# Kernel optimization log

Measured on AMD Instinct MI355X. Metric: run time of the kernel, lower is better.

## Reference

```python
import jax, jax.numpy as jnp
import numpy as np

KERNEL = (9, 9, 9)  # box-filter window
KSIZE = KERNEL[0] * KERNEL[1] * KERNEL[2]  # 729
GAMMA = 1.0


def _box_sum(x):
    # x: [B, C, D, H, W] -> channel-sum then 9x9x9 sliding-window sum (SAME pad),
    # exactly matching F.conv3d with an all-ones [1, C, 9,9,9] kernel, pad=4.
    s = jnp.sum(x, axis=1, keepdims=True)  # [B,1,D,H,W]
    return jax.lax.reduce_window(
        s, jnp.asarray(0.0, s.dtype), jax.lax.add,
        window_dimensions=(1, 1) + KERNEL,
        window_strides=(1, 1, 1, 1, 1),
        padding='SAME')


def setup_inputs() -> dict:
    key = jax.random.key(0)
    k1, k2, k3 = jax.random.split(key, 3)
    shape = (2, 1, 160, 160, 160)
    return {
        'input': jax.random.normal(k1, shape, dtype=jnp.float32),
        'target': jax.random.normal(k2, shape, dtype=jnp.float32),
        'flow': jax.random.normal(k3, shape, dtype=jnp.float32),
    }


def reference(input, target, flow):
    # normalize target from (-1, 1) to (0, 1)
    target = (target + 1.0) * 0.5
    w = jax.nn.sigmoid(flow) ** GAMMA  # voxel-wise confidence weight

    T_sum = _box_sum(target)
    I_sum = _box_sum(input)
    TT_sum = _box_sum(target * target)
    II_sum = _box_sum(input * input)
    IT_sum = _box_sum(input * target)

    Ihat = I_sum / KSIZE
    That = T_sum / KSIZE
    cross = IT_sum - Ihat * T_sum - That * I_sum + That * Ihat * KSIZE
    T_var = TT_sum - 2.0 * That * T_sum + That * That * KSIZE
    I_var = II_sum - 2.0 * Ihat * I_sum + Ihat * Ihat * KSIZE

    cc = cross * cross * w / (T_var * I_var + 1e-5)
    return -1.0 * jnp.mean(cc)
```

## Files before the change

### kernel.cpp

```cpp
#include <hip/hip_runtime.h>


constexpr int NB = 2;
constexpr int ND = 160;
constexpr int NH = 160;
constexpr int NW = 160;
constexpr int TH = 16;
constexpr int TW = 16;
constexpr int DCHUNK = 32;
constexpr int NDCH = ND / DCHUNK;
constexpr float INV_K = 1.0f / 729.0f;
constexpr double INV_COUNT = 1.0 / (double(NB) * ND * NH * NW);

__device__ __forceinline__ void compute_plane(
    const float* __restrict__ in, const float* __restrict__ tg,
    int b, int dp, int h0, int w0, int tid,
    float* __restrict__ inT, float* __restrict__ tgT,
    float* __restrict__ tmp5, float* __restrict__ Pbuf)
{
    if (tid < 144) {
        int r = tid / 6;
        int q = tid - r * 6;
        int gh = h0 - 4 + r;
        int gw = w0 - 4 + q * 4;
        float4 iv = make_float4(0.f, 0.f, 0.f, 0.f);
        float4 tv = make_float4(0.f, 0.f, 0.f, 0.f);
        if (((unsigned)gh < (unsigned)NH) && ((unsigned)gw < (unsigned)NW)) {
            long base = ((long)((b * ND + dp) * NH + gh)) * NW + gw;
            iv = *reinterpret_cast<const float4*>(in + base);
            float4 rv = *reinterpret_cast<const float4*>(tg + base);
            tv.x = fmaf(rv.x, 0.5f, 0.5f);
            tv.y = fmaf(rv.y, 0.5f, 0.5f);
            tv.z = fmaf(rv.z, 0.5f, 0.5f);
            tv.w = fmaf(rv.w, 0.5f, 0.5f);
        }
        reinterpret_cast<float4*>(inT)[r * 6 + q] = iv;
        reinterpret_cast<float4*>(tgT)[r * 6 + q] = tv;
    }
    __syncthreads();

    {
        int pos = tid;
        #pragma unroll
        for (int rep = 0; rep < 2; ++rep) {
            if (pos < 384) {
                int r = pos >> 4, wo = pos & 15;
                const float* ir = inT + r * 24 + wo;
                const float* tr = tgT + r * 24 + wo;
                float s0 = 0.f, s1 = 0.f, s2 = 0.f, s3 = 0.f, s4 = 0.f;
                #pragma unroll
                for (int k = 0; k < 9; ++k) {
                    float ivv = ir[k];
                    float t = tr[k];
                    s0 += t;
                    s1 += ivv;
                    s2 = fmaf(t, t, s2);
                    s3 = fmaf(ivv, ivv, s3);
                    s4 = fmaf(ivv, t, s4);
                }
                int o = r * 16 + wo;
                tmp5[0 * 384 + o] = s0;
                tmp5[1 * 384 + o] = s1;
                tmp5[2 * 384 + o] = s2;
                tmp5[3 * 384 + o] = s3;
                tmp5[4 * 384 + o] = s4;
            }
            pos += 256;
        }
    }
    __syncthreads();

    if (tid < 80) {
        int f = tid >> 4, w = tid & 15;
        const float* basep = tmp5 + f * 384 + w;
        float s = 0.f;
        #pragma unroll
        for (int r = 0; r < 8; ++r) s += basep[r * 16];
        #pragma unroll
        for (int ho = 0; ho < 16; ++ho) {
            s += basep[(ho + 8) * 16];
            Pbuf[f * 256 + ho * 16 + w] = s;
            s -= basep[ho * 16];
        }
    }
    __syncthreads();
}

__global__ void __launch_bounds__(256)
cc3d_main(const float* __restrict__ in, const float* __restrict__ tg,
          const float* __restrict__ fl, double* __restrict__ acc_out)
{
    __shared__ float inT[24 * 24];
    __shared__ float tgT[24 * 24];
    __shared__ float tmp5[5 * 24 * 16];
    __shared__ float Pbuf[5 * 16 * 16];
    __shared__ float red[4];

    const int tid = threadIdx.x;
    const int w0 = blockIdx.x * TW;
    const int h0 = blockIdx.y * TH;
    const int bz = blockIdx.z;
    const int b  = bz / NDCH;
    const int d0 = (bz - b * NDCH) * DCHUNK;

    float ring[45];
    #pragma unroll
    for (int i = 0; i < 45; ++i) ring[i] = 0.f;
    float S[5] = {0.f, 0.f, 0.f, 0.f, 0.f};
    float acc = 0.f;

    #pragma unroll
    for (int l = 0; l < 8; ++l) {
        int dp = d0 - 4 + l;
        bool valid = (dp >= 0);
        if (valid) compute_plane(in, tg, b, dp, h0, w0, tid, inT, tgT, tmp5, Pbuf);
        #pragma unroll
        for (int f = 0; f < 5; ++f) {
            float pv = valid ? Pbuf[f * 256 + tid] : 0.f;
            ring[f * 9 + l] = pv;
            S[f] += pv;
        }
    }

    for (int jbase = 0; jbase < DCHUNK; jbase += 9) {
        #pragma unroll
        for (int jj = 0; jj < 9; ++jj) {
            int j = jbase + jj;
            if (j < DCHUNK) {
                int dout = d0 + j;
                int dp = dout + 4;
                bool valid = (dp < ND);
                if (valid) compute_plane(in, tg, b, dp, h0, w0, tid, inT, tgT, tmp5, Pbuf);
                const int slot = (jj + 8) % 9;
                #pragma unroll
                for (int f = 0; f < 5; ++f) {
                    float pn = valid ? Pbuf[f * 256 + tid] : 0.f;
                    S[f] += pn - ring[f * 9 + slot];
                    ring[f * 9 + slot] = pn;
                }
                int hh = tid >> 4, ww = tid & 15;
                long fidx = ((long)((b * ND + dout) * NH + (h0 + hh))) * NW + (w0 + ww);
                float x = fl[fidx];
                float wgt = 1.0f / (1.0f + __expf(-x));
                float Ts = S[0], Is = S[1], TTs = S[2], IIs = S[3], ITs = S[4];
                float Ihat = Is * INV_K;
                float That = Ts * INV_K;
                float cross = ITs - Ihat * Ts - That * Is + That * Ihat * 729.0f;
                float T_var = TTs - 2.0f * That * Ts + That * That * 729.0f;
                float I_var = IIs - 2.0f * Ihat * Is + Ihat * Ihat * 729.0f;
                float cc = cross * cross * wgt / (T_var * I_var + 1e-5f);
                acc += cc;
            }
        }
    }

    #pragma unroll
    for (int off = 32; off > 0; off >>= 1) acc += __shfl_down(acc, off);
    if ((tid & 63) == 0) red[tid >> 6] = acc;
    __syncthreads();
    if (tid == 0) {
        double v = (double)red[0] + (double)red[1] + (double)red[2] + (double)red[3];
        atomicAdd(acc_out, v);
    }
}

__global__ void cc3d_finalize(const double* __restrict__ acc, float* __restrict__ out)
{
    out[0] = (float)(-(acc[0] * INV_COUNT));
}

extern "C" void kernel_launch(void* const* d_in, const int* in_sizes, int n_in,
                              void* d_out, int out_size, void* d_ws, size_t ws_size,
                              hipStream_t stream)
{
    const float* in = (const float*)d_in[0];
    const float* tg = (const float*)d_in[1];
    const float* fl = (const float*)d_in[2];
    float* out = (float*)d_out;
    double* acc = (double*)d_ws;

    hipMemsetAsync(d_ws, 0, sizeof(double), stream);

    dim3 grid(NW / TW, NH / TH, NB * NDCH);
    cc3d_main<<<grid, dim3(256), 0, stream>>>(in, tg, fl, acc);
    cc3d_finalize<<<1, 1, 0, stream>>>(acc, out);
}
```

Before: 185.2 us.

## Prefetch next plane into registers, shrink depth chunk, fuse finalize into main kernel

Global loads for the next depth plane (input, target, flow) are now issued into registers before the current plane's shared-memory work, so load latency overlaps compute. The depth chunk drops from 32 to 20, giving more blocks and better occupancy at the cost of more halo recomputation (28 planes per 20 outputs). The H-direction sliding sum becomes a direct 9-tap sum done by all threads instead of 80, and the separate finalize kernel is replaced by a last-block-done counter with atomics. The ring buffer indexing was reorganised to match.

```diff
diff --git a/kernel.cpp b/kernel.cpp
--- a/kernel.cpp
+++ b/kernel.cpp
@@ -1,94 +1,20 @@
 #include <hip/hip_runtime.h>
 
 
-constexpr int NB = 2;
-constexpr int ND = 160;
-constexpr int NH = 160;
-constexpr int NW = 160;
-constexpr int TH = 16;
-constexpr int TW = 16;
-constexpr int DCHUNK = 32;
+constexpr int NB = 2, ND = 160, NH = 160, NW = 160;
+constexpr int TH = 16, TW = 16;
+constexpr int DCHUNK = 20;
 constexpr int NDCH = ND / DCHUNK;
+constexpr int NPLANES = DCHUNK + 8;
+constexpr int NBLOCKS = (NW / TW) * (NH / TH) * NB * NDCH;
 constexpr float INV_K = 1.0f / 729.0f;
 constexpr double INV_COUNT = 1.0 / (double(NB) * ND * NH * NW);
-
-__device__ __forceinline__ void compute_plane(
-    const float* __restrict__ in, const float* __restrict__ tg,
-    int b, int dp, int h0, int w0, int tid,
-    float* __restrict__ inT, float* __restrict__ tgT,
-    float* __restrict__ tmp5, float* __restrict__ Pbuf)
-{
-    if (tid < 144) {
-        int r = tid / 6;
-        int q = tid - r * 6;
-        int gh = h0 - 4 + r;
-        int gw = w0 - 4 + q * 4;
-        float4 iv = make_float4(0.f, 0.f, 0.f, 0.f);
-        float4 tv = make_float4(0.f, 0.f, 0.f, 0.f);
-        if (((unsigned)gh < (unsigned)NH) && ((unsigned)gw < (unsigned)NW)) {
-            long base = ((long)((b * ND + dp) * NH + gh)) * NW + gw;
-            iv = *reinterpret_cast<const float4*>(in + base);
-            float4 rv = *reinterpret_cast<const float4*>(tg + base);
-            tv.x = fmaf(rv.x, 0.5f, 0.5f);
-            tv.y = fmaf(rv.y, 0.5f, 0.5f);
-            tv.z = fmaf(rv.z, 0.5f, 0.5f);
-            tv.w = fmaf(rv.w, 0.5f, 0.5f);
-        }
-        reinterpret_cast<float4*>(inT)[r * 6 + q] = iv;
-        reinterpret_cast<float4*>(tgT)[r * 6 + q] = tv;
-    }
-    __syncthreads();
-
-    {
-        int pos = tid;
-        #pragma unroll
-        for (int rep = 0; rep < 2; ++rep) {
-            if (pos < 384) {
-                int r = pos >> 4, wo = pos & 15;
-                const float* ir = inT + r * 24 + wo;
-                const float* tr = tgT + r * 24 + wo;
-                float s0 = 0.f, s1 = 0.f, s2 = 0.f, s3 = 0.f, s4 = 0.f;
-                #pragma unroll
-                for (int k = 0; k < 9; ++k) {
-                    float ivv = ir[k];
-                    float t = tr[k];
-                    s0 += t;
-                    s1 += ivv;
-                    s2 = fmaf(t, t, s2);
-                    s3 = fmaf(ivv, ivv, s3);
-                    s4 = fmaf(ivv, t, s4);
-                }
-                int o = r * 16 + wo;
-                tmp5[0 * 384 + o] = s0;
-                tmp5[1 * 384 + o] = s1;
-                tmp5[2 * 384 + o] = s2;
-                tmp5[3 * 384 + o] = s3;
-                tmp5[4 * 384 + o] = s4;
-            }
-            pos += 256;
-        }
-    }
-    __syncthreads();
-
-    if (tid < 80) {
-        int f = tid >> 4, w = tid & 15;
-        const float* basep = tmp5 + f * 384 + w;
-        float s = 0.f;
-        #pragma unroll
-        for (int r = 0; r < 8; ++r) s += basep[r * 16];
-        #pragma unroll
-        for (int ho = 0; ho < 16; ++ho) {
-            s += basep[(ho + 8) * 16];
-            Pbuf[f * 256 + ho * 16 + w] = s;
-            s -= basep[ho * 16];
-        }
-    }
-    __syncthreads();
-}
+constexpr long PLSTRIDE = (long)NH * NW;
 
 __global__ void __launch_bounds__(256)
 cc3d_main(const float* __restrict__ in, const float* __restrict__ tg,
-          const float* __restrict__ fl, double* __restrict__ acc_out)
+          const float* __restrict__ fl, float* __restrict__ out,
+          double* __restrict__ acc_ws, unsigned* __restrict__ cnt_ws)
 {
     __shared__ float inT[24 * 24];
     __shared__ float tgT[24 * 24];
@@ -103,53 +29,132 @@
     const int b  = bz / NDCH;
     const int d0 = (bz - b * NDCH) * DCHUNK;
 
+    const int hr = tid / 6, hq = tid - hr * 6;
+    const int gh = h0 - 4 + hr;
+    const int gw = w0 - 4 + hq * 4;
+    const bool ld_active = (tid < 144) &&
+        ((unsigned)gh < (unsigned)NH) && ((unsigned)gw < (unsigned)NW);
+    const long haloBase = (long)b * ND * PLSTRIDE + (long)gh * NW + gw;
+
+    const int hh = tid >> 4, ww = tid & 15;
+    const long flBase = (long)b * ND * PLSTRIDE + (long)(h0 + hh) * NW + (w0 + ww);
+
+    float4 pvi = make_float4(0.f, 0.f, 0.f, 0.f);
+    float4 pvt = make_float4(0.f, 0.f, 0.f, 0.f);
+    float flow_pre = 0.f;
+
     float ring[45];
     #pragma unroll
     for (int i = 0; i < 45; ++i) ring[i] = 0.f;
     float S[5] = {0.f, 0.f, 0.f, 0.f, 0.f};
     float acc = 0.f;
 
-    #pragma unroll
-    for (int l = 0; l < 8; ++l) {
-        int dp = d0 - 4 + l;
-        bool valid = (dp >= 0);
-        if (valid) compute_plane(in, tg, b, dp, h0, w0, tid, inT, tgT, tmp5, Pbuf);
-        #pragma unroll
-        for (int f = 0; f < 5; ++f) {
-            float pv = valid ? Pbuf[f * 256 + tid] : 0.f;
-            ring[f * 9 + l] = pv;
-            S[f] += pv;
+    {
+        int dp = d0 - 4;
+        if (ld_active && dp >= 0) {
+            const float* pi = in + haloBase + (long)dp * PLSTRIDE;
+            const float* pt = tg + haloBase + (long)dp * PLSTRIDE;
+            pvi = *reinterpret_cast<const float4*>(pi);
+            pvt = *reinterpret_cast<const float4*>(pt);
         }
     }
 
-    for (int jbase = 0; jbase < DCHUNK; jbase += 9) {
+    for (int pbase = 0; pbase < NPLANES; pbase += 9) {
         #pragma unroll
         for (int jj = 0; jj < 9; ++jj) {
-            int j = jbase + jj;
-            if (j < DCHUNK) {
-                int dout = d0 + j;
-                int dp = dout + 4;
-                bool valid = (dp < ND);
-                if (valid) compute_plane(in, tg, b, dp, h0, w0, tid, inT, tgT, tmp5, Pbuf);
-                const int slot = (jj + 8) % 9;
+            const int p = pbase + jj;
+            if (p < NPLANES) {
+                const int dp = d0 - 4 + p;
+                const bool vald = (dp >= 0) && (dp < ND);
+
+                const float flow_cur = flow_pre;
+
+                if (vald && tid < 144) {
+                    float4 wi, wt;
+                    if (ld_active) {
+                        wi = pvi;
+                        wt.x = fmaf(pvt.x, 0.5f, 0.5f);
+                        wt.y = fmaf(pvt.y, 0.5f, 0.5f);
+                        wt.z = fmaf(pvt.z, 0.5f, 0.5f);
+                        wt.w = fmaf(pvt.w, 0.5f, 0.5f);
+                    } else {
+                        wi = make_float4(0.f, 0.f, 0.f, 0.f);
+                        wt = make_float4(0.f, 0.f, 0.f, 0.f);
+                    }
+                    reinterpret_cast<float4*>(inT)[tid] = wi;
+                    reinterpret_cast<float4*>(tgT)[tid] = wt;
+                }
+
+                if (p + 1 < NPLANES) {
+                    const int dpn = dp + 1;
+                    if (ld_active && dpn >= 0 && dpn < ND) {
+                        const float* pi = in + haloBase + (long)dpn * PLSTRIDE;
+                        const float* pt = tg + haloBase + (long)dpn * PLSTRIDE;
+                        pvi = *reinterpret_cast<const float4*>(pi);
+                        pvt = *reinterpret_cast<const float4*>(pt);
+                    }
+                    if (p >= 7) {
+                        flow_pre = fl[flBase + (long)(d0 + p - 7) * PLSTRIDE];
+                    }
+                }
+
+                if (vald) {
+                    __syncthreads();
+                    #pragma unroll
+                    for (int rep = 0; rep < 2; ++rep) {
+                        const int idx = tid + rep * 256;
+                        if (idx < 384) {
+                            const int rr = idx >> 4, wo = idx & 15;
+                            const float* ir = inT + rr * 24 + wo;
+                            const float* tr = tgT + rr * 24 + wo;
+                            float s0 = 0.f, s1 = 0.f, s2 = 0.f, s3 = 0.f, s4 = 0.f;
+                            #pragma unroll
+                            for (int k = 0; k < 9; ++k) {
+                                const float iv = ir[k];
+                                const float t  = tr[k];
+                                s0 += t;
+                                s1 += iv;
+                                s2 = fmaf(t,  t,  s2);
+                                s3 = fmaf(iv, iv, s3);
+                                s4 = fmaf(iv, t,  s4);
+                            }
+                            const int o = rr * 16 + wo;
+                            tmp5[o]          = s0;
+                            tmp5[384 + o]    = s1;
+                            tmp5[768 + o]    = s2;
+                            tmp5[1152 + o]   = s3;
+                            tmp5[1536 + o]   = s4;
+                        }
+                    }
+                    __syncthreads();
+                    #pragma unroll
+                    for (int f = 0; f < 5; ++f) {
+                        const float* bp = tmp5 + f * 384 + hh * 16 + ww;
+                        float s = 0.f;
+                        #pragma unroll
+                        for (int r9 = 0; r9 < 9; ++r9) s += bp[r9 * 16];
+                        Pbuf[f * 256 + tid] = s;
+                    }
+                    __syncthreads();
+                }
+
                 #pragma unroll
                 for (int f = 0; f < 5; ++f) {
-                    float pn = valid ? Pbuf[f * 256 + tid] : 0.f;
-                    S[f] += pn - ring[f * 9 + slot];
-                    ring[f * 9 + slot] = pn;
+                    const float pn = vald ? Pbuf[f * 256 + tid] : 0.f;
+                    S[f] += pn - ring[jj * 5 + f];
+                    ring[jj * 5 + f] = pn;
                 }
-                int hh = tid >> 4, ww = tid & 15;
-                long fidx = ((long)((b * ND + dout) * NH + (h0 + hh))) * NW + (w0 + ww);
-                float x = fl[fidx];
-                float wgt = 1.0f / (1.0f + __expf(-x));
-                float Ts = S[0], Is = S[1], TTs = S[2], IIs = S[3], ITs = S[4];
-                float Ihat = Is * INV_K;
-                float That = Ts * INV_K;
-                float cross = ITs - Ihat * Ts - That * Is + That * Ihat * 729.0f;
-                float T_var = TTs - 2.0f * That * Ts + That * That * 729.0f;
-                float I_var = IIs - 2.0f * Ihat * Is + Ihat * Ihat * 729.0f;
-                float cc = cross * cross * wgt / (T_var * I_var + 1e-5f);
-                acc += cc;
+
+                if (p >= 8) {
+                    const float wgt = 1.0f / (1.0f + __expf(-flow_cur));
+                    const float Ts = S[0], Is = S[1], TTs = S[2], IIs = S[3], ITs = S[4];
+                    const float Ihat = Is * INV_K;
+                    const float That = Ts * INV_K;
+                    const float cross = ITs - Ihat * Ts - That * Is + That * Ihat * 729.0f;
+                    const float T_var = TTs - 2.0f * That * Ts + That * That * 729.0f;
+                    const float I_var = IIs - 2.0f * Ihat * Is + Ihat * Ihat * 729.0f;
+                    acc += cross * cross * wgt / (T_var * I_var + 1e-5f);
+                }
             }
         }
     }
@@ -159,14 +164,16 @@
     if ((tid & 63) == 0) red[tid >> 6] = acc;
     __syncthreads();
     if (tid == 0) {
-        double v = (double)red[0] + (double)red[1] + (double)red[2] + (double)red[3];
-        atomicAdd(acc_out, v);
+        const double v = (double)red[0] + (double)red[1] + (double)red[2] + (double)red[3];
+        atomicAdd(acc_ws, v);
+        __threadfence();
+        const unsigned done = atomicAdd(cnt_ws, 1u);
+        if (done == (unsigned)(NBLOCKS - 1)) {
+            __threadfence();
+            const double a = atomicAdd(acc_ws, 0.0);
+            out[0] = (float)(-(a * INV_COUNT));
+        }
     }
-}
-
-__global__ void cc3d_finalize(const double* __restrict__ acc, float* __restrict__ out)
-{
-    out[0] = (float)(-(acc[0] * INV_COUNT));
 }
 
 extern "C" void kernel_launch(void* const* d_in, const int* in_sizes, int n_in,
@@ -178,10 +185,10 @@
     const float* fl = (const float*)d_in[2];
     float* out = (float*)d_out;
     double* acc = (double*)d_ws;
+    unsigned* cnt = (unsigned*)((char*)d_ws + 8);
 
-    hipMemsetAsync(d_ws, 0, sizeof(double), stream);
+    hipMemsetAsync(d_ws, 0, 16, stream);
 
     dim3 grid(NW / TW, NH / TH, NB * NDCH);
-    cc3d_main<<<grid, dim3(256), 0, stream>>>(in, tg, fl, acc);
-    cc3d_finalize<<<1, 1, 0, stream>>>(acc, out);
+    cc3d_main<<<grid, dim3(256), 0, stream>>>(in, tg, fl, out, acc, cnt);
 }
```

Result: slower. 249.6 us (+34.8%).

## Halve depth chunk, pad tmp5 stride, fold finalize into last-block reduction

Applied to the files above, without the earlier changes.

Reduces the depth chunk per block from 32 to 16, doubling the grid to 2000 blocks for better CU occupancy, at the cost of more redundant halo plane computation (8 extra planes per 16 instead of per 32). Pads the tmp5 feature stride to 385 to shift shared-memory bank mapping between features. Removes the separate finalize kernel launch by having the last block (via an atomic counter) write the final mean.

```diff
diff --git a/kernel.cpp b/kernel.cpp
--- a/kernel.cpp
+++ b/kernel.cpp
@@ -1,16 +1,14 @@
 #include <hip/hip_runtime.h>
 
 
-constexpr int NB = 2;
-constexpr int ND = 160;
-constexpr int NH = 160;
-constexpr int NW = 160;
-constexpr int TH = 16;
-constexpr int TW = 16;
-constexpr int DCHUNK = 32;
+constexpr int NB = 2, ND = 160, NH = 160, NW = 160;
+constexpr int TH = 16, TW = 16;
+constexpr int DCHUNK = 16;
 constexpr int NDCH = ND / DCHUNK;
+constexpr int NBLOCKS = (NW / TW) * (NH / TH) * NB * NDCH;
 constexpr float INV_K = 1.0f / 729.0f;
 constexpr double INV_COUNT = 1.0 / (double(NB) * ND * NH * NW);
+constexpr int T5S = 385;
 
 __device__ __forceinline__ void compute_plane(
     const float* __restrict__ in, const float* __restrict__ tg,
@@ -59,11 +57,11 @@
                     s4 = fmaf(ivv, t, s4);
                 }
                 int o = r * 16 + wo;
-                tmp5[0 * 384 + o] = s0;
-                tmp5[1 * 384 + o] = s1;
-                tmp5[2 * 384 + o] = s2;
-                tmp5[3 * 384 + o] = s3;
-                tmp5[4 * 384 + o] = s4;
+                tmp5[0 * T5S + o] = s0;
+                tmp5[1 * T5S + o] = s1;
+                tmp5[2 * T5S + o] = s2;
+                tmp5[3 * T5S + o] = s3;
+                tmp5[4 * T5S + o] = s4;
             }
             pos += 256;
         }
@@ -72,7 +70,7 @@
 
     if (tid < 80) {
         int f = tid >> 4, w = tid & 15;
-        const float* basep = tmp5 + f * 384 + w;
+        const float* basep = tmp5 + f * T5S + w;
         float s = 0.f;
         #pragma unroll
         for (int r = 0; r < 8; ++r) s += basep[r * 16];
@@ -88,12 +86,13 @@
 
 __global__ void __launch_bounds__(256)
 cc3d_main(const float* __restrict__ in, const float* __restrict__ tg,
-          const float* __restrict__ fl, double* __restrict__ acc_out)
+          const float* __restrict__ fl, float* __restrict__ out,
+          double* __restrict__ acc_ws, unsigned* __restrict__ cnt_ws)
 {
     __shared__ float inT[24 * 24];
     __shared__ float tgT[24 * 24];
-    __shared__ float tmp5[5 * 24 * 16];
-    __shared__ float Pbuf[5 * 16 * 16];
+    __shared__ float tmp5[5 * T5S];
+    __shared__ float Pbuf[5 * 256];
     __shared__ float red[4];
 
     const int tid = threadIdx.x;
@@ -159,14 +158,16 @@
     if ((tid & 63) == 0) red[tid >> 6] = acc;
     __syncthreads();
     if (tid == 0) {
-        double v = (double)red[0] + (double)red[1] + (double)red[2] + (double)red[3];
-        atomicAdd(acc_out, v);
+        const double v = (double)red[0] + (double)red[1] + (double)red[2] + (double)red[3];
+        atomicAdd(acc_ws, v);
+        __threadfence();
+        const unsigned done = atomicAdd(cnt_ws, 1u);
+        if (done == (unsigned)(NBLOCKS - 1)) {
+            __threadfence();
+            const double a = atomicAdd(acc_ws, 0.0);
+            out[0] = (float)(-(a * INV_COUNT));
+        }
     }
-}
-
-__global__ void cc3d_finalize(const double* __restrict__ acc, float* __restrict__ out)
-{
-    out[0] = (float)(-(acc[0] * INV_COUNT));
 }
 
 extern "C" void kernel_launch(void* const* d_in, const int* in_sizes, int n_in,
@@ -178,10 +179,10 @@
     const float* fl = (const float*)d_in[2];
     float* out = (float*)d_out;
     double* acc = (double*)d_ws;
+    unsigned* cnt = (unsigned*)((char*)d_ws + 8);
 
-    hipMemsetAsync(d_ws, 0, sizeof(double), stream);
+    hipMemsetAsync(d_ws, 0, 16, stream);
 
     dim3 grid(NW / TW, NH / TH, NB * NDCH);
-    cc3d_main<<<grid, dim3(256), 0, stream>>>(in, tg, fl, acc);
-    cc3d_finalize<<<1, 1, 0, stream>>>(acc, out);
+    cc3d_main<<<grid, dim3(256), 0, stream>>>(in, tg, fl, out, acc, cnt);
 }
```

Result: slower. 255.3 us (+37.8%).
